# Optimization experiments

Hardware: AMD Instinct MI355X
Metric: run time of the kernel (lower is better)

The kernel has to match this reference:

```python
import jax, jax.numpy as jnp
import numpy as np

V, H, L, B, S, T = 32000, 256, 4, 32, 64, 64


def setup_inputs() -> dict:
    key = jax.random.key(0)
    ks = jax.random.split(key, 16)
    sc = 0.05
    return {
        "encoder_outputs": jax.random.normal(ks[0], (B, S, H), jnp.float32),
        "encoder_hidden": jax.random.normal(ks[1], (L, B, H), jnp.float32),
        "decoder_input": jax.random.randint(ks[2], (B, T), 0, V),
        "embedding": jax.random.normal(ks[3], (V, H), jnp.float32) * sc,
        "Wa": jax.random.normal(ks[4], (H, H * L), jnp.float32) * sc,
        "bWa": jnp.zeros((H,), jnp.float32),
        "Ua": jax.random.normal(ks[5], (H, H), jnp.float32) * sc,
        "bUa": jnp.zeros((H,), jnp.float32),
        "Va": jax.random.normal(ks[6], (1, H), jnp.float32) * sc,
        "bVa": jnp.zeros((1,), jnp.float32),
        "W_ih0": jax.random.normal(ks[7], (3 * H, 2 * H), jnp.float32) * sc,
        "W_ih_rest": jax.random.normal(ks[8], (L - 1, 3 * H, H), jnp.float32) * sc,
        "W_hh": jax.random.normal(ks[9], (L, 3 * H, H), jnp.float32) * sc,
        "b_ih": jnp.zeros((L, 3 * H), jnp.float32),
        "b_hh": jnp.zeros((L, 3 * H), jnp.float32),
        "W_out": jax.random.normal(ks[10], (V, H), jnp.float32) * sc,
        "b_out": jnp.zeros((V,), jnp.float32),
    }


def _gru_cell(x, h, W_ih, W_hh, b_ih, b_hh):
    # PyTorch gate order: r, z, n
    gi = x @ W_ih.T + b_ih  # [B, 3H]
    gh = h @ W_hh.T + b_hh  # [B, 3H]
    ir, iz, inn = jnp.split(gi, 3, axis=-1)
    hr, hz, hn = jnp.split(gh, 3, axis=-1)
    r = jax.nn.sigmoid(ir + hr)
    z = jax.nn.sigmoid(iz + hz)
    n = jnp.tanh(inn + r * hn)
    return (1.0 - z) * n + z * h


def reference(encoder_outputs, encoder_hidden, decoder_input, embedding,
              Wa, bWa, Ua, bUa, Va, bVa,
              W_ih0, W_ih_rest, W_hh, b_ih, b_hh, W_out, b_out):
    keys = encoder_outputs  # [B,S,H]
    UaK = keys @ Ua.T + bUa  # precompute Ua(keys): [B,S,H]
    nlayers = W_hh.shape[0]

    def step(hidden, tok):
        # hidden: [L,B,H], tok: [B]
        emb = embedding[tok]  # [B,H]
        query = jnp.transpose(hidden, (1, 0, 2)).reshape(hidden.shape[1], -1)  # [B, L*H]
        e = jnp.tanh((query @ Wa.T + bWa)[:, None, :] + UaK)  # [B,S,H]
        scores = jnp.squeeze(e @ Va.T + bVa, -1)  # [B,S]
        w = jax.nn.softmax(scores, axis=-1)  # [B,S]
        ctx = jnp.einsum('bs,bsh->bh', w, keys)  # [B,H]
        x = jnp.concatenate([emb, ctx], axis=-1)  # [B,2H]
        new_h = []
        for l in range(nlayers):
            Wih = W_ih0 if l == 0 else W_ih_rest[l - 1]
            h_l = _gru_cell(x, hidden[l], Wih, W_hh[l], b_ih[l], b_hh[l])
            new_h.append(h_l)
            x = h_l
        logits = x @ W_out.T + b_out  # [B,V]
        return jnp.stack(new_h, 0), (logits, w)

    hidden_final, (logits_tbv, attn_tbs) = jax.lax.scan(step, encoder_hidden, decoder_input.T)
    logits = jnp.transpose(logits_tbv, (1, 0, 2))  # [B,T,V]
    attentions = jnp.transpose(attn_tbs, (1, 0, 2))  # [B,T,S]
    return jax.nn.log_softmax(logits, axis=-1), hidden_final, attentions
```

## Files before the change

### kernel.cpp

```cpp
#include <hip/hip_runtime.h>

typedef short s16x8 __attribute__((ext_vector_type(8)));
typedef float f32x4 __attribute__((ext_vector_type(4)));
typedef _Float16 h2 __attribute__((ext_vector_type(2)));
typedef unsigned u32x4 __attribute__((ext_vector_type(4)));
typedef unsigned u32x2 __attribute__((ext_vector_type(2)));

static __device__ __forceinline__ unsigned short f2bf(float f){
  unsigned u = __builtin_bit_cast(unsigned, f);
  unsigned r = (u + 0x7fffu + ((u >> 16) & 1u)) >> 16;
  return (unsigned short)r;
}
static __device__ __forceinline__ float sigm(float x){
  return __builtin_amdgcn_rcpf(1.f + __expf(-x));
}
static __device__ __forceinline__ float tanh_(float x){
  float e = __expf(2.f * x);
  return 1.f - 2.f * __builtin_amdgcn_rcpf(e + 1.f);
}
static __device__ __forceinline__ unsigned pk2(float a, float b){
  h2 h = { (_Float16)a, (_Float16)b };
  return __builtin_bit_cast(unsigned, h);
}
static __device__ __forceinline__ h2 bch2(unsigned u){
  return __builtin_bit_cast(h2, u);
}
static __device__ __forceinline__ float dot2(unsigned x, unsigned w, float acc){
  return __builtin_amdgcn_fdot2(bch2(x), bch2(w), acc, false);
}

__global__ void k_tr(const float* __restrict__ in, float* __restrict__ out, int R, int C, int ld){
  int i = blockIdx.x * 256 + threadIdx.x;
  if (i >= R * C) return;
  int c = i / R, r = i - c * R;
  out[i] = in[r * ld + c];
}

__global__ void k_wbpack(const float* __restrict__ W, unsigned short* __restrict__ Wb){
  int p = blockIdx.x * 256 + threadIdx.x;
  int j = p & 7, l = (p >> 3) & 63, ks = (p >> 9) & 7, nt = p >> 12;
  int v = nt * 16 + (l & 15);
  int k = ks * 32 + ((l >> 4) << 3) + j;
  Wb[p] = f2bf(W[v * 256 + k]);
}

__global__ void k_packW(const float* __restrict__ src, unsigned short* __restrict__ dst,
                        int ld, int k0){
  int idx = blockIdx.x * 256 + threadIdx.x;
  int g = idx >> 8, k = idx & 255;
  int cs = g / 24, c = g - cs * 24;
  _Float16 v = (_Float16)src[g * ld + k0 + k];
  dst[cs * 6144 + (k >> 1) * 48 + c * 2 + (k & 1)] = __builtin_bit_cast(unsigned short, v);
}

__global__ void k_packWa(const float* __restrict__ Wa, unsigned short* __restrict__ dst){
  int idx = blockIdx.x * 256 + threadIdx.x;
  int c = idx >> 10, kk = idx & 1023;
  int l = kk >> 8, k = kk & 255;
  int cs = c >> 3, c8 = c & 7;
  _Float16 v = (_Float16)Wa[c * 1024 + kk];
  dst[(l * 32 + cs) * 2048 + (k >> 1) * 16 + c8 * 2 + (k & 1)] = __builtin_bit_cast(unsigned short, v);
}

__global__ void k_uak(const float* __restrict__ keys, const float* __restrict__ UaT,
                      const float* __restrict__ bUa, float* __restrict__ UaK){
  __shared__ float kl[256];
  int row = blockIdx.x, tid = threadIdx.x;
  kl[tid] = keys[row * 256 + tid];
  __syncthreads();
  float acc = bUa[tid];
  #pragma unroll 8
  for (int k = 0; k < 256; ++k) acc += kl[k] * UaT[k * 256 + tid];
  UaK[row * 256 + tid] = acc;
}

__global__ void k_gie(const int* __restrict__ tok, const float* __restrict__ emb,
                      const float* __restrict__ W0eT, const float* __restrict__ bih,
                      float* __restrict__ giE){
  __shared__ float el[256];
  int blk = blockIdx.x;
  int t = blk >> 5, b = blk & 31, tid = threadIdx.x;
  int tk = tok[b * 64 + t];
  el[tid] = emb[tk * 256 + tid];
  __syncthreads();
  for (int g = tid; g < 768; g += 256){
    float acc = bih[g];
    #pragma unroll 8
    for (int k = 0; k < 256; ++k) acc += el[k] * W0eT[k * 768 + g];
    giE[blk * 768 + g] = acc;
  }
}

static __device__ __forceinline__ void gridbar(int* bar, int* epoch){
  __syncthreads();
  if (threadIdx.x == 0){
    ++(*epoch);
    __hip_atomic_fetch_add(bar, 1, __ATOMIC_ACQ_REL, __HIP_MEMORY_SCOPE_AGENT);
    const int target = 32 * (*epoch);
    while (__hip_atomic_load(bar, __ATOMIC_ACQUIRE, __HIP_MEMORY_SCOPE_AGENT) < target)
      __builtin_amdgcn_s_sleep(2);
  }
  __syncthreads();
}

__launch_bounds__(512, 1)
__global__ void k_rec(const float* __restrict__ keys, const float* __restrict__ ehid,
                      const unsigned short* __restrict__ WaP,
                      const unsigned short* __restrict__ WhhP,
                      const unsigned short* __restrict__ WihP,
                      const float* __restrict__ bWa, const float* __restrict__ Va,
                      const float* __restrict__ bVa,
                      const float* __restrict__ UaK, const float* __restrict__ giE,
                      const float* __restrict__ bih, const float* __restrict__ bhh,
                      float* __restrict__ qWgP, unsigned* __restrict__ ghgP,
                      unsigned* __restrict__ gigP, unsigned* __restrict__ ctx2g,
                      int* __restrict__ bar,
                      unsigned short* __restrict__ Xb, float* __restrict__ outH,
                      float* __restrict__ outA)
{
  __shared__ unsigned Hpk[32][4][132];
  __shared__ unsigned Cpk[32][128];
  __shared__ float vlds[256];
  __shared__ float qWl[256];
  __shared__ float sc[64], watt[64];
  __shared__ float ctxl[256];
  __shared__ float red[512];
  const int cs = blockIdx.x;
  const int tid = threadIdx.x;

  for (int i = tid; i < 16384; i += 512){
    int l = i >> 12, b = (i >> 7) & 31, kp = i & 127;
    const float* hp = ehid + l * 8192 + b * 256 + 2 * kp;
    Hpk[b][l][kp] = pk2(hp[0], hp[1]);
  }
  if (tid < 256) vlds[tid] = Va[tid];
  __syncthreads();

  int epoch = 0;
  for (int t = 0; t < 64; ++t){
    const int tp = t & 1;
    #pragma unroll
    for (int pass = 0; pass < 2; ++pass){
      const int u = pass * 512 + tid;
      const int b = u >> 5, m = u & 31;
      float a0, a1, a2, a3;
      const unsigned short* wb;
      int l, c0, wstep;
      if (m < 8){
        l = m >> 1; const int cg = m & 1;
        wb = WaP + (l * 32 + cs) * 2048 + cg * 8;
        wstep = 16; c0 = cs * 8 + cg * 4;
        a0 = a1 = a2 = a3 = 0.f;
      } else {
        const int mm = m - 8; l = mm / 6; const int cg = mm - l * 6;
        wb = WhhP + (l * 32 + cs) * 6144 + cg * 8;
        wstep = 48; c0 = cs * 24 + cg * 4;
        const float4 bb = *(const float4*)(bhh + l * 768 + c0);
        a0 = bb.x; a1 = bb.y; a2 = bb.z; a3 = bb.w;
      }
      const unsigned* xp = &Hpk[b][l][0];
      #pragma unroll 8
      for (int kp = 0; kp < 128; ++kp){
        u32x4 w = *(const u32x4*)(wb + kp * wstep);
        unsigned x = xp[kp];
        a0 = dot2(x, w.x, a0); a1 = dot2(x, w.y, a1);
        a2 = dot2(x, w.z, a2); a3 = dot2(x, w.w, a3);
      }
      if (m < 8){
        *(f32x4*)(qWgP + (b * 4 + l) * 256 + c0) = (f32x4){a0, a1, a2, a3};
      } else {
        u32x2 o = { pk2(a0, a1), pk2(a2, a3) };
        *(u32x2*)(ghgP + tp * 49152 + (l * 32 + b) * 384 + (c0 >> 1)) = o;
      }
    }
    gridbar(bar, &epoch);

    if (tid < 256){
      qWl[tid] = qWgP[(cs * 4 + 0) * 256 + tid] + qWgP[(cs * 4 + 1) * 256 + tid]
               + qWgP[(cs * 4 + 2) * 256 + tid] + qWgP[(cs * 4 + 3) * 256 + tid] + bWa[tid];
    }
    __syncthreads();
    {
      int s = tid >> 3, p = tid & 7;
      const float* up = UaK + ((cs << 6) + s) * 256 + p * 32;
      const float* qp = qWl + p * 32;
      const float* vp = vlds + p * 32;
      float acc = 0.f;
      #pragma unroll 8
      for (int i = 0; i < 32; ++i) acc += vp[i] * tanh_(qp[i] + up[i]);
      acc += __shfl_xor(acc, 1, 64);
      acc += __shfl_xor(acc, 2, 64);
      acc += __shfl_xor(acc, 4, 64);
      if (p == 0) sc[s] = acc + bVa[0];
    }
    __syncthreads();
    if (tid < 64){
      float v = sc[tid];
      float m2 = v;
      #pragma unroll
      for (int off = 1; off < 64; off <<= 1) m2 = fmaxf(m2, __shfl_xor(m2, off, 64));
      float e = __expf(v - m2);
      float ssum = e;
      #pragma unroll
      for (int off = 1; off < 64; off <<= 1) ssum += __shfl_xor(ssum, off, 64);
      float w = e * __builtin_amdgcn_rcpf(ssum);
      watt[tid] = w;
      outA[(cs * 64 + t) * 64 + tid] = w;
    }
    __syncthreads();
    {
      int o = tid & 255, p = tid >> 8;
      const float* kp2 = keys + (cs * 64 + p * 32) * 256 + o;
      float acc = 0.f;
      #pragma unroll 8
      for (int s2 = 0; s2 < 32; ++s2) acc += watt[p * 32 + s2] * kp2[s2 * 256];
      red[tid] = acc;
    }
    __syncthreads();
    if (tid < 256) ctxl[tid] = red[tid] + red[256 + tid];
    __syncthreads();
    if (tid < 128) ctx2g[cs * 128 + tid] = pk2(ctxl[2 * tid], ctxl[2 * tid + 1]);
    gridbar(bar, &epoch);

    for (int i = tid; i < 4096; i += 512) Cpk[i >> 7][i & 127] = ctx2g[i];
    __syncthreads();

    const int tb = t * 32;
    for (int l = 0; l < 4; ++l){
      if (tid < 192){
        const int b = tid / 6, cg = tid - b * 6;
        const int c0 = cs * 24 + cg * 4;
        const unsigned short* wb = WihP + (l * 32 + cs) * 6144 + cg * 8;
        float a0, a1, a2, a3;
        if (l == 0){
          const float4 bb = *(const float4*)(giE + (tb + b) * 768 + c0);
          a0 = bb.x; a1 = bb.y; a2 = bb.z; a3 = bb.w;
        } else {
          const float4 bb = *(const float4*)(bih + l * 768 + c0);
          a0 = bb.x; a1 = bb.y; a2 = bb.z; a3 = bb.w;
        }
        const unsigned* xp = (l == 0) ? &Cpk[b][0] : &Hpk[b][l - 1][0];
        #pragma unroll 8
        for (int kp = 0; kp < 128; ++kp){
          u32x4 w = *(const u32x4*)(wb + kp * 48);
          unsigned x = xp[kp];
          a0 = dot2(x, w.x, a0); a1 = dot2(x, w.y, a1);
          a2 = dot2(x, w.z, a2); a3 = dot2(x, w.w, a3);
        }
        u32x2 o = { pk2(a0, a1), pk2(a2, a3) };
        *(u32x2*)(gigP + l * 12288 + b * 384 + (c0 >> 1)) = o;
      }
      gridbar(bar, &epoch);
      const unsigned* gl = gigP + l * 12288;
      const unsigned* gh = ghgP + tp * 49152 + l * 32 * 384;
      #pragma unroll
      for (int i2 = 0; i2 < 8; ++i2){
        const int u = tid + i2 * 512;
        const int b = u >> 7, kp = u & 127;
        h2 gir = bch2(gl[b * 384 + kp]);
        h2 giz = bch2(gl[b * 384 + 128 + kp]);
        h2 gin = bch2(gl[b * 384 + 256 + kp]);
        h2 ghr = bch2(gh[b * 384 + kp]);
        h2 ghz = bch2(gh[b * 384 + 128 + kp]);
        h2 ghn = bch2(gh[b * 384 + 256 + kp]);
        h2 hp = bch2(Hpk[b][l][kp]);
        float hn0, hn1;
        {
          float r = sigm((float)gir[0] + (float)ghr[0]);
          float z = sigm((float)giz[0] + (float)ghz[0]);
          float n = tanh_((float)gin[0] + r * (float)ghn[0]);
          hn0 = (1.f - z) * n + z * (float)hp[0];
        }
        {
          float r = sigm((float)gir[1] + (float)ghr[1]);
          float z = sigm((float)giz[1] + (float)ghz[1]);
          float n = tanh_((float)gin[1] + r * (float)ghn[1]);
          hn1 = (1.f - z) * n + z * (float)hp[1];
        }
        Hpk[b][l][kp] = pk2(hn0, hn1);
        if (l == 3 && b == cs)
          *(unsigned*)(Xb + (cs * 64 + t) * 256 + 2 * kp) =
              (unsigned)f2bf(hn0) | ((unsigned)f2bf(hn1) << 16);
        if (t == 63 && b == cs){
          outH[l * 8192 + cs * 256 + 2 * kp]     = hn0;
          outH[l * 8192 + cs * 256 + 2 * kp + 1] = hn1;
        }
      }
      __syncthreads();
    }
  }
}

__launch_bounds__(512)
__global__ void k_g1(const unsigned short* __restrict__ Xb, const unsigned short* __restrict__ Wb,
                     const float* __restrict__ bout, float* __restrict__ Spart)
{
  const int mt = blockIdx.x, nc = blockIdx.y;
  const int tid = threadIdx.x, lane = tid & 63, wv = tid >> 6;
  const int c = lane & 15, q = lane >> 4;
  const int r0 = mt * 64;
  s16x8 afr[4][8];
  #pragma unroll
  for (int rt = 0; rt < 4; ++rt){
    const unsigned short* xp = Xb + (r0 + rt * 16 + c) * 256 + q * 8;
    #pragma unroll
    for (int ks = 0; ks < 8; ++ks) afr[rt][ks] = *(const s16x8*)(xp + ks * 32);
  }
  float ssum[4][4];
  #pragma unroll
  for (int rt = 0; rt < 4; ++rt){ ssum[rt][0]=0.f; ssum[rt][1]=0.f; ssum[rt][2]=0.f; ssum[rt][3]=0.f; }
  const int ntEnd = nc * 250 + 250;
  for (int nt = nc * 250 + wv; nt < ntEnd; nt += 8){
    const unsigned short* wp = Wb + nt * 4096 + lane * 8;
    f32x4 acc[4];
    #pragma unroll
    for (int rt = 0; rt < 4; ++rt) acc[rt] = (f32x4){0.f, 0.f, 0.f, 0.f};
    #pragma unroll
    for (int ks = 0; ks < 8; ++ks){
      s16x8 bfr = *(const s16x8*)(wp + ks * 512);
      #pragma unroll
      for (int rt = 0; rt < 4; ++rt)
        acc[rt] = __builtin_amdgcn_mfma_f32_16x16x32_bf16(afr[rt][ks], bfr, acc[rt], 0, 0, 0);
    }
    float bo = bout[nt * 16 + c];
    #pragma unroll
    for (int rt = 0; rt < 4; ++rt){
      #pragma unroll
      for (int i = 0; i < 4; ++i) ssum[rt][i] += __expf(acc[rt][i] + bo);
    }
  }
  #pragma unroll
  for (int off = 1; off < 16; off <<= 1){
    #pragma unroll
    for (int rt = 0; rt < 4; ++rt){
      #pragma unroll
      for (int i = 0; i < 4; ++i) ssum[rt][i] += __shfl_xor(ssum[rt][i], off, 64);
    }
  }
  __shared__ float lred[8][64];
  if (c == 0){
    #pragma unroll
    for (int rt = 0; rt < 4; ++rt){
      #pragma unroll
      for (int i = 0; i < 4; ++i) lred[wv][rt * 16 + q * 4 + i] = ssum[rt][i];
    }
  }
  __syncthreads();
  if (tid < 64){
    float s = 0.f;
    #pragma unroll
    for (int w = 0; w < 8; ++w) s += lred[w][tid];
    Spart[(r0 + tid) * 8 + nc] = s;
  }
}

__global__ void k_g1b(const float* __restrict__ Spart, float* __restrict__ Z){
  int r = blockIdx.x * 256 + threadIdx.x;
  float s = 0.f;
  #pragma unroll
  for (int nc = 0; nc < 8; ++nc) s += Spart[r * 8 + nc];
  Z[r] = __logf(s);
}

__launch_bounds__(512)
__global__ void k_g2(const unsigned short* __restrict__ Xb, const unsigned short* __restrict__ Wb,
                     const float* __restrict__ bout, const float* __restrict__ Z,
                     float* __restrict__ out)
{
  const int mt = blockIdx.x, nc = blockIdx.y;
  const int tid = threadIdx.x, lane = tid & 63, wv = tid >> 6;
  const int c = lane & 15, q = lane >> 4;
  const int r0 = mt * 64;
  s16x8 afr[4][8];
  #pragma unroll
  for (int rt = 0; rt < 4; ++rt){
    const unsigned short* xp = Xb + (r0 + rt * 16 + c) * 256 + q * 8;
    #pragma unroll
    for (int ks = 0; ks < 8; ++ks) afr[rt][ks] = *(const s16x8*)(xp + ks * 32);
  }
  float zr[4][4];
  #pragma unroll
  for (int rt = 0; rt < 4; ++rt){
    #pragma unroll
    for (int i = 0; i < 4; ++i) zr[rt][i] = Z[r0 + rt * 16 + q * 4 + i];
  }
  const int ntEnd = nc * 250 + 250;
  for (int nt = nc * 250 + wv; nt < ntEnd; nt += 8){
    const unsigned short* wp = Wb + nt * 4096 + lane * 8;
    f32x4 acc[4];
    #pragma unroll
    for (int rt = 0; rt < 4; ++rt) acc[rt] = (f32x4){0.f, 0.f, 0.f, 0.f};
    #pragma unroll
    for (int ks = 0; ks < 8; ++ks){
      s16x8 bfr = *(const s16x8*)(wp + ks * 512);
      #pragma unroll
      for (int rt = 0; rt < 4; ++rt)
        acc[rt] = __builtin_amdgcn_mfma_f32_16x16x32_bf16(afr[rt][ks], bfr, acc[rt], 0, 0, 0);
    }
    float bo = bout[nt * 16 + c];
    #pragma unroll
    for (int rt = 0; rt < 4; ++rt){
      #pragma unroll
      for (int i = 0; i < 4; ++i)
        out[(r0 + rt * 16 + q * 4 + i) * 32000 + nt * 16 + c] = acc[rt][i] + bo - zr[rt][i];
    }
  }
}

extern "C" void kernel_launch(void* const* d_in, const int* in_sizes, int n_in,
                              void* d_out, int out_size, void* d_ws, size_t ws_size,
                              hipStream_t stream)
{
  const float* keys = (const float*)d_in[0];
  const float* ehid = (const float*)d_in[1];
  const int*   dinp = (const int*)d_in[2];
  const float* emb  = (const float*)d_in[3];
  const float* Wa   = (const float*)d_in[4];
  const float* bWa  = (const float*)d_in[5];
  const float* Ua   = (const float*)d_in[6];
  const float* bUa  = (const float*)d_in[7];
  const float* Va   = (const float*)d_in[8];
  const float* bVa  = (const float*)d_in[9];
  const float* Wih0 = (const float*)d_in[10];
  const float* Wihr = (const float*)d_in[11];
  const float* Whh  = (const float*)d_in[12];
  const float* bih  = (const float*)d_in[13];
  const float* bhh  = (const float*)d_in[14];
  const float* Wout = (const float*)d_in[15];
  const float* bout = (const float*)d_in[16];

  char* p = (char*)d_ws;
  auto alloc = [&](size_t n){ char* r = p; p += (n + 255) & ~(size_t)255; return r; };
  unsigned short* WaP  = (unsigned short*)alloc(262144 * 2);
  unsigned short* WhhP = (unsigned short*)alloc(786432 * 2);
  unsigned short* WihP = (unsigned short*)alloc(786432 * 2);
  float* UaT   = (float*)alloc(65536 * 4);
  float* W0eT  = (float*)alloc(196608 * 4);
  float* UaK   = (float*)alloc(524288 * 4);
  float* giE   = (float*)alloc(1572864 * 4);
  unsigned short* Xb = (unsigned short*)alloc(524288 * 2);
  unsigned short* Wb = (unsigned short*)alloc(8192000 * 2);
  float* Spart = (float*)alloc(16384 * 4);
  float* Zr    = (float*)alloc(2048 * 4);
  float* qWgP  = (float*)alloc(32768 * 4);
  unsigned* ghgP = (unsigned*)alloc(98304 * 4);
  unsigned* gigP = (unsigned*)alloc(49152 * 4);
  unsigned* ctx2g = (unsigned*)alloc(4096 * 4);
  int* bar = (int*)alloc(256);

  float* outL = (float*)d_out;
  float* outH = outL + 65536000;
  float* outA = outH + 32768;

  k_tr<<<256, 256, 0, stream>>>(Ua,   UaT,  256, 256, 256);
  k_tr<<<768, 256, 0, stream>>>(Wih0, W0eT, 768, 256, 512);

  k_packWa<<<1024, 256, 0, stream>>>(Wa, WaP);
  for (int l = 0; l < 4; ++l)
    k_packW<<<768, 256, 0, stream>>>(Whh + l * 196608, WhhP + l * 196608, 256, 0);
  k_packW<<<768, 256, 0, stream>>>(Wih0, WihP, 512, 256);
  for (int l = 1; l < 4; ++l)
    k_packW<<<768, 256, 0, stream>>>(Wihr + (l - 1) * 196608, WihP + l * 196608, 256, 0);

  k_wbpack<<<32000, 256, 0, stream>>>(Wout, Wb);
  k_uak<<<2048, 256, 0, stream>>>(keys, UaT, bUa, UaK);
  k_gie<<<2048, 256, 0, stream>>>(dinp, emb, W0eT, bih, giE);

  hipMemsetAsync(bar, 0, 256, stream);

  k_rec<<<32, 512, 0, stream>>>(keys, ehid, WaP, WhhP, WihP, bWa, Va, bVa,
                                UaK, giE, bih, bhh,
                                qWgP, ghgP, gigP, ctx2g, bar, Xb, outH, outA);

  k_g1<<<dim3(32, 8), 512, 0, stream>>>(Xb, Wb, bout, Spart);
  k_g1b<<<8, 256, 0, stream>>>(Spart, Zr);
  k_g2<<<dim3(32, 8), 512, 0, stream>>>(Xb, Wb, bout, Zr, outL);
}
```

Measured before the change: 5.120 ms.

## Use MFMA for recurrent GRU matmuls with per-layer block groups

```diff
diff --git a/kernel.cpp b/kernel.cpp
--- a/kernel.cpp
+++ b/kernel.cpp
@@ -1,10 +1,8 @@
 #include <hip/hip_runtime.h>
 
 typedef short s16x8 __attribute__((ext_vector_type(8)));
+typedef _Float16 f16x8 __attribute__((ext_vector_type(8)));
 typedef float f32x4 __attribute__((ext_vector_type(4)));
-typedef _Float16 h2 __attribute__((ext_vector_type(2)));
-typedef unsigned u32x4 __attribute__((ext_vector_type(4)));
-typedef unsigned u32x2 __attribute__((ext_vector_type(2)));
 
 static __device__ __forceinline__ unsigned short f2bf(float f){
   unsigned u = __builtin_bit_cast(unsigned, f);
@@ -17,16 +15,6 @@
 static __device__ __forceinline__ float tanh_(float x){
   float e = __expf(2.f * x);
   return 1.f - 2.f * __builtin_amdgcn_rcpf(e + 1.f);
-}
-static __device__ __forceinline__ unsigned pk2(float a, float b){
-  h2 h = { (_Float16)a, (_Float16)b };
-  return __builtin_bit_cast(unsigned, h);
-}
-static __device__ __forceinline__ h2 bch2(unsigned u){
-  return __builtin_bit_cast(h2, u);
-}
-static __device__ __forceinline__ float dot2(unsigned x, unsigned w, float acc){
-  return __builtin_amdgcn_fdot2(bch2(x), bch2(w), acc, false);
 }
 
 __global__ void k_tr(const float* __restrict__ in, float* __restrict__ out, int R, int C, int ld){
@@ -44,22 +32,34 @@
   Wb[p] = f2bf(W[v * 256 + k]);
 }
 
-__global__ void k_packW(const float* __restrict__ src, unsigned short* __restrict__ dst,
-                        int ld, int k0){
-  int idx = blockIdx.x * 256 + threadIdx.x;
-  int g = idx >> 8, k = idx & 255;
-  int cs = g / 24, c = g - cs * 24;
-  _Float16 v = (_Float16)src[g * ld + k0 + k];
-  dst[cs * 6144 + (k >> 1) * 48 + c * 2 + (k & 1)] = __builtin_bit_cast(unsigned short, v);
-}
-
-__global__ void k_packWa(const float* __restrict__ Wa, unsigned short* __restrict__ dst){
-  int idx = blockIdx.x * 256 + threadIdx.x;
-  int c = idx >> 10, kk = idx & 1023;
-  int l = kk >> 8, k = kk & 255;
-  int cs = c >> 3, c8 = c & 7;
-  _Float16 v = (_Float16)Wa[c * 1024 + kk];
-  dst[(l * 32 + cs) * 2048 + (k >> 1) * 16 + c8 * 2 + (k & 1)] = __builtin_bit_cast(unsigned short, v);
+__global__ void k_wpackA(const float* __restrict__ Whh, _Float16* __restrict__ dst){
+  int p = blockIdx.x * 256 + threadIdx.x;
+  int j = p & 7, lane = (p >> 3) & 63, ks = (p >> 9) & 7, tile = p >> 12;
+  int l = tile / 48, nt = tile - l * 48;
+  int row = nt * 16 + (lane & 15);
+  int k = ks * 32 + ((lane >> 4) << 3) + j;
+  dst[p] = (_Float16)Whh[l * 196608 + row * 256 + k];
+}
+
+__global__ void k_wpackQ(const float* __restrict__ Wa, _Float16* __restrict__ dst){
+  int p = blockIdx.x * 256 + threadIdx.x;
+  int j = p & 7, lane = (p >> 3) & 63, ks = (p >> 9) & 7, tile = p >> 12;
+  int kc = tile >> 4, nt = tile & 15;
+  int row = nt * 16 + (lane & 15);
+  int k = ks * 32 + ((lane >> 4) << 3) + j;
+  dst[p] = (_Float16)Wa[row * 1024 + kc * 256 + k];
+}
+
+__global__ void k_wpackI(const float* __restrict__ Wih0, const float* __restrict__ Wihr,
+                         _Float16* __restrict__ dst){
+  int p = blockIdx.x * 256 + threadIdx.x;
+  int j = p & 7, lane = (p >> 3) & 63, ks = (p >> 9) & 7, tile = p >> 12;
+  int l = tile / 48, nt = tile - l * 48;
+  int row = nt * 16 + (lane & 15);
+  int k = ks * 32 + ((lane >> 4) << 3) + j;
+  float v = (l == 0) ? Wih0[row * 512 + 256 + k]
+                     : Wihr[(l - 1) * 196608 + row * 256 + k];
+  dst[p] = (_Float16)v;
 }
 
 __global__ void k_uak(const float* __restrict__ keys, const float* __restrict__ UaT,
@@ -98,86 +98,94 @@
     __hip_atomic_fetch_add(bar, 1, __ATOMIC_ACQ_REL, __HIP_MEMORY_SCOPE_AGENT);
     const int target = 32 * (*epoch);
     while (__hip_atomic_load(bar, __ATOMIC_ACQUIRE, __HIP_MEMORY_SCOPE_AGENT) < target)
-      __builtin_amdgcn_s_sleep(2);
+      __builtin_amdgcn_s_sleep(1);
   }
   __syncthreads();
 }
 
 __launch_bounds__(512, 1)
 __global__ void k_rec(const float* __restrict__ keys, const float* __restrict__ ehid,
-                      const unsigned short* __restrict__ WaP,
-                      const unsigned short* __restrict__ WhhP,
-                      const unsigned short* __restrict__ WihP,
+                      const _Float16* __restrict__ WpkA, const _Float16* __restrict__ WpkQ,
+                      const _Float16* __restrict__ WpkI,
                       const float* __restrict__ bWa, const float* __restrict__ Va,
                       const float* __restrict__ bVa,
                       const float* __restrict__ UaK, const float* __restrict__ giE,
                       const float* __restrict__ bih, const float* __restrict__ bhh,
-                      float* __restrict__ qWgP, unsigned* __restrict__ ghgP,
-                      unsigned* __restrict__ gigP, unsigned* __restrict__ ctx2g,
+                      float* __restrict__ qWg, _Float16* __restrict__ ghg,
+                      _Float16* __restrict__ gig, _Float16* __restrict__ ctxg,
                       int* __restrict__ bar,
                       unsigned short* __restrict__ Xb, float* __restrict__ outH,
                       float* __restrict__ outA)
 {
-  __shared__ unsigned Hpk[32][4][132];
-  __shared__ unsigned Cpk[32][128];
-  __shared__ float vlds[256];
+  __shared__ _Float16 hl[32][264];
+  __shared__ float vlds[256], bWal[256];
+  __shared__ float bihl[768], bhhl[768];
   __shared__ float qWl[256];
   __shared__ float sc[64], watt[64];
   __shared__ float ctxl[256];
   __shared__ float red[512];
-  const int cs = blockIdx.x;
-  const int tid = threadIdx.x;
-
-  for (int i = tid; i < 16384; i += 512){
-    int l = i >> 12, b = (i >> 7) & 31, kp = i & 127;
-    const float* hp = ehid + l * 8192 + b * 256 + 2 * kp;
-    Hpk[b][l][kp] = pk2(hp[0], hp[1]);
-  }
-  if (tid < 256) vlds[tid] = Va[tid];
+
+  const int cs = blockIdx.x, tid = threadIdx.x;
+  const int gl = cs >> 3;
+  const int gidx = cs & 7;
+  const int wv = tid >> 6, lane = tid & 63;
+  const int fc = lane & 15, fq = lane >> 4;
+
+  for (int i = tid; i < 8192; i += 512){
+    int b = i >> 8, k = i & 255;
+    hl[b][k] = (_Float16)ehid[gl * 8192 + b * 256 + k];
+  }
+  if (tid < 256){ vlds[tid] = Va[tid]; bWal[tid] = bWa[tid]; }
+  for (int i = tid; i < 768; i += 512){
+    bihl[i] = bih[gl * 768 + i];
+    bhhl[i] = bhh[gl * 768 + i];
+  }
   __syncthreads();
 
   int epoch = 0;
   for (int t = 0; t < 64; ++t){
-    const int tp = t & 1;
-    #pragma unroll
-    for (int pass = 0; pass < 2; ++pass){
-      const int u = pass * 512 + tid;
-      const int b = u >> 5, m = u & 31;
-      float a0, a1, a2, a3;
-      const unsigned short* wb;
-      int l, c0, wstep;
-      if (m < 8){
-        l = m >> 1; const int cg = m & 1;
-        wb = WaP + (l * 32 + cs) * 2048 + cg * 8;
-        wstep = 16; c0 = cs * 8 + cg * 4;
-        a0 = a1 = a2 = a3 = 0.f;
+
+    {
+      f16x8 afr0[8], afr1[8];
+      #pragma unroll
+      for (int ks = 0; ks < 8; ++ks){
+        afr0[ks] = *(const f16x8*)&hl[fc][ks * 32 + fq * 8];
+        afr1[ks] = *(const f16x8*)&hl[16 + fc][ks * 32 + fq * 8];
+      }
+      const _Float16* bp = (wv < 6)
+          ? (WpkA + (gl * 48 + gidx * 6 + wv) * 4096)
+          : (WpkQ + (gl * 16 + gidx * 2 + (wv - 6)) * 4096);
+      f32x4 ac0 = {0.f,0.f,0.f,0.f}, ac1 = {0.f,0.f,0.f,0.f};
+      #pragma unroll
+      for (int ks = 0; ks < 8; ++ks){
+        f16x8 bfr = *(const f16x8*)(bp + ks * 512 + lane * 8);
+        ac0 = __builtin_amdgcn_mfma_f32_16x16x32_f16(afr0[ks], bfr, ac0, 0, 0, 0);
+        ac1 = __builtin_amdgcn_mfma_f32_16x16x32_f16(afr1[ks], bfr, ac1, 0, 0, 0);
+      }
+      if (wv < 6){
+        const int c0 = (gidx * 6 + wv) * 16 + fc;
+        _Float16* dst = ghg + (gl * 32) * 768 + c0;
+        #pragma unroll
+        for (int i = 0; i < 4; ++i){
+          dst[(fq * 4 + i) * 768]        = (_Float16)ac0[i];
+          dst[(16 + fq * 4 + i) * 768]   = (_Float16)ac1[i];
+        }
       } else {
-        const int mm = m - 8; l = mm / 6; const int cg = mm - l * 6;
-        wb = WhhP + (l * 32 + cs) * 6144 + cg * 8;
-        wstep = 48; c0 = cs * 24 + cg * 4;
-        const float4 bb = *(const float4*)(bhh + l * 768 + c0);
-        a0 = bb.x; a1 = bb.y; a2 = bb.z; a3 = bb.w;
-      }
-      const unsigned* xp = &Hpk[b][l][0];
-      #pragma unroll 8
-      for (int kp = 0; kp < 128; ++kp){
-        u32x4 w = *(const u32x4*)(wb + kp * wstep);
-        unsigned x = xp[kp];
-        a0 = dot2(x, w.x, a0); a1 = dot2(x, w.y, a1);
-        a2 = dot2(x, w.z, a2); a3 = dot2(x, w.w, a3);
-      }
-      if (m < 8){
-        *(f32x4*)(qWgP + (b * 4 + l) * 256 + c0) = (f32x4){a0, a1, a2, a3};
-      } else {
-        u32x2 o = { pk2(a0, a1), pk2(a2, a3) };
-        *(u32x2*)(ghgP + tp * 49152 + (l * 32 + b) * 384 + (c0 >> 1)) = o;
+        const int c0 = (gidx * 2 + (wv - 6)) * 16 + fc;
+        float* dst = qWg + (gl * 32) * 256 + c0;
+        #pragma unroll
+        for (int i = 0; i < 4; ++i){
+          dst[(fq * 4 + i) * 256]        = ac0[i];
+          dst[(16 + fq * 4 + i) * 256]   = ac1[i];
+        }
       }
     }
     gridbar(bar, &epoch);
 
     if (tid < 256){
-      qWl[tid] = qWgP[(cs * 4 + 0) * 256 + tid] + qWgP[(cs * 4 + 1) * 256 + tid]
-               + qWgP[(cs * 4 + 2) * 256 + tid] + qWgP[(cs * 4 + 3) * 256 + tid] + bWa[tid];
+      qWl[tid] = qWg[(0 * 32 + cs) * 256 + tid] + qWg[(1 * 32 + cs) * 256 + tid]
+               + qWg[(2 * 32 + cs) * 256 + tid] + qWg[(3 * 32 + cs) * 256 + tid]
+               + bWal[tid];
     }
     __syncthreads();
     {
@@ -217,77 +225,101 @@
       red[tid] = acc;
     }
     __syncthreads();
-    if (tid < 256) ctxl[tid] = red[tid] + red[256 + tid];
-    __syncthreads();
-    if (tid < 128) ctx2g[cs * 128 + tid] = pk2(ctxl[2 * tid], ctxl[2 * tid + 1]);
+    if (tid < 256){
+      ctxl[tid] = red[tid] + red[256 + tid];
+      ctxg[cs * 256 + tid] = (_Float16)ctxl[tid];
+    }
     gridbar(bar, &epoch);
 
-    for (int i = tid; i < 4096; i += 512) Cpk[i >> 7][i & 127] = ctx2g[i];
-    __syncthreads();
-
-    const int tb = t * 32;
-    for (int l = 0; l < 4; ++l){
-      if (tid < 192){
-        const int b = tid / 6, cg = tid - b * 6;
-        const int c0 = cs * 24 + cg * 4;
-        const unsigned short* wb = WihP + (l * 32 + cs) * 6144 + cg * 8;
-        float a0, a1, a2, a3;
-        if (l == 0){
-          const float4 bb = *(const float4*)(giE + (tb + b) * 768 + c0);
-          a0 = bb.x; a1 = bb.y; a2 = bb.z; a3 = bb.w;
+    auto do_gi = [&](int l, const _Float16* xg){
+      f16x8 afr0[8], afr1[8];
+      #pragma unroll
+      for (int ks = 0; ks < 8; ++ks){
+        if (xg){
+          afr0[ks] = *(const f16x8*)(xg + fc * 256 + ks * 32 + fq * 8);
+          afr1[ks] = *(const f16x8*)(xg + (16 + fc) * 256 + ks * 32 + fq * 8);
         } else {
-          const float4 bb = *(const float4*)(bih + l * 768 + c0);
-          a0 = bb.x; a1 = bb.y; a2 = bb.z; a3 = bb.w;
+          afr0[ks] = *(const f16x8*)&hl[fc][ks * 32 + fq * 8];
+          afr1[ks] = *(const f16x8*)&hl[16 + fc][ks * 32 + fq * 8];
         }
-        const unsigned* xp = (l == 0) ? &Cpk[b][0] : &Hpk[b][l - 1][0];
-        #pragma unroll 8
-        for (int kp = 0; kp < 128; ++kp){
-          u32x4 w = *(const u32x4*)(wb + kp * 48);
-          unsigned x = xp[kp];
-          a0 = dot2(x, w.x, a0); a1 = dot2(x, w.y, a1);
-          a2 = dot2(x, w.z, a2); a3 = dot2(x, w.w, a3);
-        }
-        u32x2 o = { pk2(a0, a1), pk2(a2, a3) };
-        *(u32x2*)(gigP + l * 12288 + b * 384 + (c0 >> 1)) = o;
-      }
-      gridbar(bar, &epoch);
-      const unsigned* gl = gigP + l * 12288;
-      const unsigned* gh = ghgP + tp * 49152 + l * 32 * 384;
-      #pragma unroll
-      for (int i2 = 0; i2 < 8; ++i2){
-        const int u = tid + i2 * 512;
-        const int b = u >> 7, kp = u & 127;
-        h2 gir = bch2(gl[b * 384 + kp]);
-        h2 giz = bch2(gl[b * 384 + 128 + kp]);
-        h2 gin = bch2(gl[b * 384 + 256 + kp]);
-        h2 ghr = bch2(gh[b * 384 + kp]);
-        h2 ghz = bch2(gh[b * 384 + 128 + kp]);
-        h2 ghn = bch2(gh[b * 384 + 256 + kp]);
-        h2 hp = bch2(Hpk[b][l][kp]);
-        float hn0, hn1;
+      }
+      const _Float16* bp = WpkI + (l * 48 + gidx * 6 + wv) * 4096;
+      f32x4 ac0 = {0.f,0.f,0.f,0.f}, ac1 = {0.f,0.f,0.f,0.f};
+      #pragma unroll
+      for (int ks = 0; ks < 8; ++ks){
+        f16x8 bfr = *(const f16x8*)(bp + ks * 512 + lane * 8);
+        ac0 = __builtin_amdgcn_mfma_f32_16x16x32_f16(afr0[ks], bfr, ac0, 0, 0, 0);
+        ac1 = __builtin_amdgcn_mfma_f32_16x16x32_f16(afr1[ks], bfr, ac1, 0, 0, 0);
+      }
+      const int c0 = (gidx * 6 + wv) * 16 + fc;
+      _Float16* dst = gig + l * 24576 + c0;
+      #pragma unroll
+      for (int i = 0; i < 4; ++i){
+        dst[(fq * 4 + i) * 768]      = (_Float16)ac0[i];
+        dst[(16 + fq * 4 + i) * 768] = (_Float16)ac1[i];
+      }
+    };
+
+    auto do_gates = [&](int l){
+      const int b = tid >> 4, kq = (tid & 15) << 4;
+      const _Float16* gp = gig + l * 24576 + b * 768 + kq;
+      const _Float16* hp = ghg + (l * 32 + b) * 768 + kq;
+      const float* gep = giE + (t * 32 + b) * 768 + kq;
+      f16x8 gr0 = *(const f16x8*)(gp);       f16x8 gr1 = *(const f16x8*)(gp + 8);
+      f16x8 gz0 = *(const f16x8*)(gp + 256); f16x8 gz1 = *(const f16x8*)(gp + 264);
+      f16x8 gn0 = *(const f16x8*)(gp + 512); f16x8 gn1 = *(const f16x8*)(gp + 520);
+      f16x8 hr0 = *(const f16x8*)(hp);       f16x8 hr1 = *(const f16x8*)(hp + 8);
+      f16x8 hz0 = *(const f16x8*)(hp + 256); f16x8 hz1 = *(const f16x8*)(hp + 264);
+      f16x8 hn0 = *(const f16x8*)(hp + 512); f16x8 hn1 = *(const f16x8*)(hp + 520);
+      f16x8 ho0 = *(const f16x8*)&hl[b][kq];
+      f16x8 ho1 = *(const f16x8*)&hl[b][kq + 8];
+      f16x8 o0, o1;
+      const bool mine = ((b >> 2) == gidx);
+      #pragma unroll
+      for (int i = 0; i < 8; ++i){
         {
-          float r = sigm((float)gir[0] + (float)ghr[0]);
-          float z = sigm((float)giz[0] + (float)ghz[0]);
-          float n = tanh_((float)gin[0] + r * (float)ghn[0]);
-          hn0 = (1.f - z) * n + z * (float)hp[0];
+          float giR = (float)gr0[i] + (l == 0 ? gep[i]       : bihl[kq + i]);
+          float giZ = (float)gz0[i] + (l == 0 ? gep[256 + i] : bihl[256 + kq + i]);
+          float giN = (float)gn0[i] + (l == 0 ? gep[512 + i] : bihl[512 + kq + i]);
+          float r = sigm(giR + (float)hr0[i] + bhhl[kq + i]);
+          float z = sigm(giZ + (float)hz0[i] + bhhl[256 + kq + i]);
+          float n = tanh_(giN + r * ((float)hn0[i] + bhhl[512 + kq + i]));
+          float hv = (1.f - z) * n + z * (float)ho0[i];
+          o0[i] = (_Float16)hv;
+          if (l == 3 && mine) Xb[(b * 64 + t) * 256 + kq + i] = f2bf(hv);
+          if (t == 63 && mine) outH[l * 8192 + b * 256 + kq + i] = hv;
         }
         {
-          float r = sigm((float)gir[1] + (float)ghr[1]);
-          float z = sigm((float)giz[1] + (float)ghz[1]);
-          float n = tanh_((float)gin[1] + r * (float)ghn[1]);
-          hn1 = (1.f - z) * n + z * (float)hp[1];
+          float giR = (float)gr1[i] + (l == 0 ? gep[8 + i]       : bihl[kq + 8 + i]);
+          float giZ = (float)gz1[i] + (l == 0 ? gep[264 + i]     : bihl[256 + kq + 8 + i]);
+          float giN = (float)gn1[i] + (l == 0 ? gep[520 + i]     : bihl[512 + kq + 8 + i]);
+          float r = sigm(giR + (float)hr1[i] + bhhl[kq + 8 + i]);
+          float z = sigm(giZ + (float)hz1[i] + bhhl[256 + kq + 8 + i]);
+          float n = tanh_(giN + r * ((float)hn1[i] + bhhl[512 + kq + 8 + i]));
+          float hv = (1.f - z) * n + z * (float)ho1[i];
+          o1[i] = (_Float16)hv;
+          if (l == 3 && mine) Xb[(b * 64 + t) * 256 + kq + 8 + i] = f2bf(hv);
+          if (t == 63 && mine) outH[l * 8192 + b * 256 + kq + 8 + i] = hv;
         }
-        Hpk[b][l][kp] = pk2(hn0, hn1);
-        if (l == 3 && b == cs)
-          *(unsigned*)(Xb + (cs * 64 + t) * 256 + 2 * kp) =
-              (unsigned)f2bf(hn0) | ((unsigned)f2bf(hn1) << 16);
-        if (t == 63 && b == cs){
-          outH[l * 8192 + cs * 256 + 2 * kp]     = hn0;
-          outH[l * 8192 + cs * 256 + 2 * kp + 1] = hn1;
-        }
-      }
-      __syncthreads();
-    }
+      }
+      *(f16x8*)&hl[b][kq] = o0;
+      *(f16x8*)&hl[b][kq + 8] = o1;
+    };
+
+    if (gl == 3 && wv < 6) do_gi(0, ctxg);
+    gridbar(bar, &epoch);
+
+    for (int lw = 0; lw < 3; ++lw){
+      if (gl == lw){
+        do_gates(lw);
+        __syncthreads();
+        if (wv < 6) do_gi(lw + 1, nullptr);
+      }
+      gridbar(bar, &epoch);
+    }
+
+    if (gl == 3) do_gates(3);
+    __syncthreads();
   }
 }
 
@@ -296,7 +328,7 @@
                      const float* __restrict__ bout, float* __restrict__ Spart)
 {
   const int mt = blockIdx.x, nc = blockIdx.y;
-  const int tid = threadIdx.x, lane = tid & 63, wv = tid >> 6;
+  const int tid = threadIdx.x, lane = tid & 63, wvv = tid >> 6;
   const int c = lane & 15, q = lane >> 4;
   const int r0 = mt * 64;
   s16x8 afr[4][8];
@@ -310,7 +342,7 @@
   #pragma unroll
   for (int rt = 0; rt < 4; ++rt){ ssum[rt][0]=0.f; ssum[rt][1]=0.f; ssum[rt][2]=0.f; ssum[rt][3]=0.f; }
   const int ntEnd = nc * 250 + 250;
-  for (int nt = nc * 250 + wv; nt < ntEnd; nt += 8){
+  for (int nt = nc * 250 + wvv; nt < ntEnd; nt += 8){
     const unsigned short* wp = Wb + nt * 4096 + lane * 8;
     f32x4 acc[4];
     #pragma unroll
@@ -342,7 +374,7 @@
     #pragma unroll
     for (int rt = 0; rt < 4; ++rt){
       #pragma unroll
-      for (int i = 0; i < 4; ++i) lred[wv][rt * 16 + q * 4 + i] = ssum[rt][i];
+      for (int i = 0; i < 4; ++i) lred[wvv][rt * 16 + q * 4 + i] = ssum[rt][i];
     }
   }
   __syncthreads();
@@ -368,7 +400,7 @@
                      float* __restrict__ out)
 {
   const int mt = blockIdx.x, nc = blockIdx.y;
-  const int tid = threadIdx.x, lane = tid & 63, wv = tid >> 6;
+  const int tid = threadIdx.x, lane = tid & 63, wvv = tid >> 6;
   const int c = lane & 15, q = lane >> 4;
   const int r0 = mt * 64;
   s16x8 afr[4][8];
@@ -385,7 +417,7 @@
     for (int i = 0; i < 4; ++i) zr[rt][i] = Z[r0 + rt * 16 + q * 4 + i];
   }
   const int ntEnd = nc * 250 + 250;
-  for (int nt = nc * 250 + wv; nt < ntEnd; nt += 8){
+  for (int nt = nc * 250 + wvv; nt < ntEnd; nt += 8){
     const unsigned short* wp = Wb + nt * 4096 + lane * 8;
     f32x4 acc[4];
     #pragma unroll
@@ -431,9 +463,9 @@
 
   char* p = (char*)d_ws;
   auto alloc = [&](size_t n){ char* r = p; p += (n + 255) & ~(size_t)255; return r; };
-  unsigned short* WaP  = (unsigned short*)alloc(262144 * 2);
-  unsigned short* WhhP = (unsigned short*)alloc(786432 * 2);
-  unsigned short* WihP = (unsigned short*)alloc(786432 * 2);
+  _Float16* WpkA = (_Float16*)alloc(786432 * 2);
+  _Float16* WpkQ = (_Float16*)alloc(262144 * 2);
+  _Float16* WpkI = (_Float16*)alloc(786432 * 2);
   float* UaT   = (float*)alloc(65536 * 4);
   float* W0eT  = (float*)alloc(196608 * 4);
   float* UaK   = (float*)alloc(524288 * 4);
@@ -442,10 +474,10 @@
   unsigned short* Wb = (unsigned short*)alloc(8192000 * 2);
   float* Spart = (float*)alloc(16384 * 4);
   float* Zr    = (float*)alloc(2048 * 4);
-  float* qWgP  = (float*)alloc(32768 * 4);
-  unsigned* ghgP = (unsigned*)alloc(98304 * 4);
-  unsigned* gigP = (unsigned*)alloc(49152 * 4);
-  unsigned* ctx2g = (unsigned*)alloc(4096 * 4);
+  float* qWg   = (float*)alloc(32768 * 4);
+  _Float16* ghg = (_Float16*)alloc(98304 * 2);
+  _Float16* gig = (_Float16*)alloc(98304 * 2);
+  _Float16* ctxg = (_Float16*)alloc(8192 * 2);
   int* bar = (int*)alloc(256);
 
   float* outL = (float*)d_out;
@@ -455,12 +487,9 @@
   k_tr<<<256, 256, 0, stream>>>(Ua,   UaT,  256, 256, 256);
   k_tr<<<768, 256, 0, stream>>>(Wih0, W0eT, 768, 256, 512);
 
-  k_packWa<<<1024, 256, 0, stream>>>(Wa, WaP);
-  for (int l = 0; l < 4; ++l)
-    k_packW<<<768, 256, 0, stream>>>(Whh + l * 196608, WhhP + l * 196608, 256, 0);
-  k_packW<<<768, 256, 0, stream>>>(Wih0, WihP, 512, 256);
-  for (int l = 1; l < 4; ++l)
-    k_packW<<<768, 256, 0, stream>>>(Wihr + (l - 1) * 196608, WihP + l * 196608, 256, 0);
+  k_wpackA<<<3072, 256, 0, stream>>>(Whh, WpkA);
+  k_wpackQ<<<1024, 256, 0, stream>>>(Wa, WpkQ);
+  k_wpackI<<<3072, 256, 0, stream>>>(Wih0, Wihr, WpkI);
 
   k_wbpack<<<32000, 256, 0, stream>>>(Wout, Wb);
   k_uak<<<2048, 256, 0, stream>>>(keys, UaT, bUa, UaK);
@@ -468,9 +497,9 @@
 
   hipMemsetAsync(bar, 0, 256, stream);
 
-  k_rec<<<32, 512, 0, stream>>>(keys, ehid, WaP, WhhP, WihP, bWa, Va, bVa,
+  k_rec<<<32, 512, 0, stream>>>(keys, ehid, WpkA, WpkQ, WpkI, bWa, Va, bVa,
                                 UaK, giE, bih, bhh,
-                                qWgP, ghgP, gigP, ctx2g, bar, Xb, outH, outA);
+                                qWg, ghg, gig, ctxg, bar, Xb, outH, outA);
 
   k_g1<<<dim3(32, 8), 512, 0, stream>>>(Xb, Wb, bout, Spart);
   k_g1b<<<8, 256, 0, stream>>>(Spart, Zr);
```

New measurement: 4.690 ms. -8.4%, faster.
